# Performance work log

Hardware: AMD Instinct MI355X
Metric: run time of the kernel (lower is better)

Reference implementation:

```python
import jax, jax.numpy as jnp
import numpy as np
from math import factorial

# ---- static config mirroring Cace.__init__ ----
MAX_L = 3            # max angular degree
N_RBF = 8            # Bessel radial basis size
RB = 8               # n_radial_basis (radial embedding dim after transform)
K = 3                # n_atom_basis -> edge channels C = K*K
NZ = 4               # len(zs)
CUTOFF = 5.5
N_NODES = 2000
N_EDGES = 50000
T_MP = 1             # num_message_passing
MP_NORM = 1.0 / np.sqrt(25.0)   # 1/sqrt(avg_num_neighbors)
C = K * K

def _lxlylz(max_l):
    out = []
    for l in range(max_l + 1):
        for lx in range(l, -1, -1):
            for ly in range(l - lx, -1, -1):
                out.append((lx, ly, l - lx - ly))
    return out

L_LIST = _lxlylz(MAX_L)                 # 20 Cartesian monomials for max_l=3
NL = len(L_LIST)
LX = np.array([t[0] for t in L_LIST]); LY = np.array([t[1] for t in L_LIST]); LZ = np.array([t[2] for t in L_LIST])
DEGS = LX + LY + LZ                     # degree l of each monomial
MULTI = np.array([factorial(int(d)) / (factorial(int(a)) * factorial(int(b)) * factorial(int(c)))
                  for a, b, c, d in zip(LX, LY, LZ, DEGS)], dtype=np.float32)
SEL = np.zeros((NL, MAX_L + 1), np.float32)
SEL[np.arange(NL), DEGS] = 1.0          # monomial -> degree one-hot (for per-l sums)
NB = 1 + (MAX_L + 1)                    # symmetrizer feats: nu=1 (l=0) + nu=2 per l

def bessel(r):  # [E] -> [E, N_RBF]
    n = jnp.arange(1, N_RBF + 1, dtype=r.dtype)
    return jnp.sqrt(2.0 / CUTOFF) * jnp.sin(n[None, :] * jnp.pi * r[:, None] / CUTOFF) / r[:, None]

def poly_cutoff(r):  # MACE-style polynomial cutoff, p=6
    p = 6.0
    u = r / CUTOFF
    f = 1.0 - (p + 1.0) * (p + 2.0) / 2.0 * u**6 + p * (p + 2.0) * u**7 - p * (p + 1.0) / 2.0 * u**8
    return f * (u < 1.0)

def axis_pows(x):  # [E] -> [E, MAX_L+1] = x^0..x^MAX_L (safe grads, handles negatives)
    pows = [jnp.ones_like(x)]
    for _ in range(MAX_L):
        pows.append(pows[-1] * x)
    return jnp.stack(pows, axis=1)

def angular(u):  # unit vectors [E,3] -> Cartesian monomials [E, NL]
    return axis_pows(u[:, 0])[:, LX] * axis_pows(u[:, 1])[:, LY] * axis_pows(u[:, 2])[:, LZ]

def radial_transform(x, W):  # x [N,R,L,C], W [MAX_L+1,R,Rb] shared per degree l
    return jnp.einsum('nrlc,lrb->nblc', x, W[DEGS])

def symmetrize(A):  # A [N,Rb,NL,C] -> B [N,Rb,NB,C]
    b1 = A[:, :, :1, :]  # nu=1: the (0,0,0) monomial (index 0)
    w = (A * A) * jnp.asarray(MULTI)[None, None, :, None]
    b2 = jnp.einsum('nrlc,lm->nrmc', w, jnp.asarray(SEL))  # nu=2 invariant per degree l
    return jnp.concatenate([b1, b2], axis=2)


def setup_inputs() -> dict:
    key = jax.random.key(0)
    ks = jax.random.split(key, 9)
    positions = jax.random.uniform(ks[0], (N_NODES, 3), dtype=jnp.float32) * 12.0
    species = jax.random.randint(ks[1], (N_NODES,), 0, NZ)
    send = jax.random.randint(ks[2], (N_EDGES,), 0, N_NODES)
    off = jax.random.randint(ks[3], (N_EDGES,), 1, N_NODES)
    recv = (send + off) % N_NODES  # no self-edges -> strictly positive edge lengths
    edge_index = jnp.stack([send, recv])
    shifts = jnp.zeros((N_EDGES, 3), jnp.float32)
    W_embed = jax.random.normal(ks[4], (NZ, K), jnp.float32)
    W_radial = jax.random.normal(ks[5], (MAX_L + 1, N_RBF, RB), jnp.float32) / np.sqrt(N_RBF)
    W_mem = jax.random.normal(ks[6], (MAX_L + 1, RB, RB), jnp.float32) / np.sqrt(RB)
    W_ar = jax.random.normal(ks[7], (N_RBF, RB), jnp.float32) / np.sqrt(N_RBF)
    W_chi = jax.random.normal(ks[8], (RB, NB), jnp.float32) * 0.1
    return {"positions": positions, "shifts": shifts, "W_embed": W_embed, "W_radial": W_radial,
            "W_mem": W_mem, "W_ar": W_ar, "W_chi": W_chi, "species": species, "edge_index": edge_index}


def reference(positions, shifts, W_embed, W_radial, W_mem, W_ar, W_chi, species, edge_index):
    n_nodes = positions.shape[0]
    send, recv = edge_index[0], edge_index[1]
    # edge geometry
    vec = positions[recv] - positions[send] + shifts
    lengths = jnp.linalg.norm(vec, axis=-1)
    u = vec / (lengths[:, None] + 1e-9)
    rad = bessel(lengths)          # [E,R]
    fcut = poly_cutoff(lengths)    # [E]
    ang = angular(u)               # [E,NL]
    # edge type encoding: outer product of sender/receiver species embeddings
    emb = W_embed[species]         # [N,K]
    enc = (emb[send][:, :, None] * emb[recv][:, None, :]).reshape(-1, C)  # [E,C]
    # elementwise_multiply_3tensors -> [E,R,NL,C]
    edge_attri = jnp.einsum('er,el,ec->erlc', rad * fcut[:, None], ang, enc)
    A = radial_transform(jax.ops.segment_sum(edge_attri, recv, num_segments=n_nodes), W_radial)  # [N,Rb,NL,C]
    B = symmetrize(A)              # [N,Rb,NB,C]
    feats = [B]
    for _ in range(T_MP):
        mem = jnp.einsum('nrlc,lrb->nblc', A, W_mem[DEGS])        # NodeMemory
        chi = jnp.einsum('nbkc,bk->nc', B, W_chi)                  # MessageBchi node scalar
        msg_bchi = edge_attri * chi[send][:, None, None, :]
        A_bchi = radial_transform(jax.ops.segment_sum(msg_bchi, recv, num_segments=n_nodes), W_radial)
        fr = (rad @ W_ar) * fcut[:, None]                          # MessageAr radial filter [E,Rb]
        msg_ar = A[send] * fr[:, :, None, None]
        A_ar = jax.ops.segment_sum(msg_ar, recv, num_segments=n_nodes)
        A = (A_ar + A_bchi) * MP_NORM + mem
        B = symmetrize(A)
        feats.append(B)
    return jnp.stack(feats, axis=-1)   # [N,Rb,NB,C,T_MP+1]
```

## Files before the change

kernel.cpp:

```cpp
#include <hip/hip_runtime.h>
#include <hip/hip_bf16.h>


#define CUTF 5.5f
#define MPNORM 0.2f

__constant__ int   d_DEGS[20]  = {0,1,1,1,2,2,2,2,2,2,3,3,3,3,3,3,3,3,3,3};
__constant__ float d_MULTI[20] = {1,1,1,1,1,2,2,1,2,1,1,3,3,3,6,3,1,3,3,1};

__global__ __launch_bounds__(1024) void k_prep(const int* __restrict__ eidx,
                                               int* __restrict__ offs,
                                               int* __restrict__ erank,
                                               int N, int E) {
  __shared__ int cnt[2048];
  __shared__ int part[1024];
  int t = threadIdx.x;
  cnt[t] = 0; cnt[t + 1024] = 0;
  __syncthreads();
  const int* recv = eidx + E;
  if ((E & 3) == 0) {
    for (int i = t * 4; i + 3 < E; i += 4096) {
      int4 v = *reinterpret_cast<const int4*>(recv + i);
      int r0 = atomicAdd(&cnt[v.x], 1);
      int r1 = atomicAdd(&cnt[v.y], 1);
      int r2 = atomicAdd(&cnt[v.z], 1);
      int r3 = atomicAdd(&cnt[v.w], 1);
      *reinterpret_cast<int4*>(erank + i) = make_int4(r0, r1, r2, r3);
    }
  } else {
    for (int i = t; i < E; i += 1024) erank[i] = atomicAdd(&cnt[recv[i]], 1);
  }
  __syncthreads();
  int a = cnt[2 * t], b = cnt[2 * t + 1];
  int s = a + b;
  part[t] = s;
  __syncthreads();
  for (int d = 1; d < 1024; d <<= 1) {
    int add = (t >= d) ? part[t - d] : 0;
    __syncthreads();
    part[t] += add;
    __syncthreads();
  }
  int excl = part[t] - s;
  if (2 * t     < N) offs[2 * t]     = excl;
  if (2 * t + 1 < N) offs[2 * t + 1] = excl + a;
  if (t == 1023) offs[N] = part[1023];
}

__global__ __launch_bounds__(64) void k_edge(
                       const float* __restrict__ pos,
                       const float* __restrict__ shifts,
                       const float* __restrict__ Wemb,
                       const float* __restrict__ War,
                       const int* __restrict__ species,
                       const int* __restrict__ eidx,
                       const int* __restrict__ offs,
                       const int* __restrict__ erank,
                       float* __restrict__ edata,
                       int* __restrict__ esend,
                       int E) {
  __shared__ float war_s[64];
  int t = threadIdx.x;
  war_s[t] = War[t];
  __syncthreads();
  int e = blockIdx.x * 64 + t;
  if (e >= E) return;
  int s  = eidx[e];
  int rI = eidx[E + e];
  int rk = erank[e];
  float vx = pos[rI*3+0] - pos[s*3+0] + shifts[e*3+0];
  float vy = pos[rI*3+1] - pos[s*3+1] + shifts[e*3+1];
  float vz = pos[rI*3+2] - pos[s*3+2] + shifts[e*3+2];
  float len = sqrtf(vx*vx + vy*vy + vz*vz);
  float inv = 1.0f / (len + 1e-9f);
  float ux = vx*inv, uy = vy*inv, uz = vz*inv;
  float uu = len * (1.0f/CUTF);
  float u2 = uu*uu, u6 = u2*u2*u2;
  float fcut = (uu < 1.0f) ? (1.0f - 28.0f*u6 + 48.0f*u6*uu - 21.0f*u6*u2) : 0.0f;
  float x = 3.14159265358979f * uu;
  float sn = sinf(x), c2 = 2.0f*cosf(x), snm1 = 0.0f;
  float pref = sqrtf(2.0f/CUTF) / (len + 1e-20f);
  float rad[8];
  float v[48];
  #pragma unroll
  for (int k = 0; k < 8; k++) {
    rad[k] = pref * sn;
    v[k]   = rad[k] * fcut;
    float nxt = c2*sn - snm1; snm1 = sn; sn = nxt;
  }
  #pragma unroll
  for (int b = 0; b < 8; b++) {
    float a = 0.0f;
    #pragma unroll
    for (int k = 0; k < 8; k++) a += rad[k] * war_s[k*8+b];
    v[8+b] = a * fcut;
  }
  float px2 = ux*ux, py2 = uy*uy, pz2 = uz*uz;
  v[16] = 1.0f; v[17] = ux;     v[18] = uy;     v[19] = uz;
  v[20] = px2;  v[21] = ux*uy;  v[22] = ux*uz;  v[23] = py2;
  v[24] = uy*uz;v[25] = pz2;
  v[26] = px2*ux; v[27] = px2*uy; v[28] = px2*uz; v[29] = ux*py2;
  v[30] = ux*uy*uz; v[31] = ux*pz2; v[32] = py2*uy; v[33] = py2*uz;
  v[34] = uy*pz2; v[35] = pz2*uz;
  int zs = species[s], zr = species[rI];
  float es0 = Wemb[zs*3+0], es1 = Wemb[zs*3+1], es2 = Wemb[zs*3+2];
  float er0 = Wemb[zr*3+0], er1 = Wemb[zr*3+1], er2 = Wemb[zr*3+2];
  v[36] = es0*er0; v[37] = es0*er1; v[38] = es0*er2;
  v[39] = es1*er0; v[40] = es1*er1; v[41] = es1*er2;
  v[42] = es2*er0; v[43] = es2*er1; v[44] = es2*er2;
  v[45] = 0.0f; v[46] = 0.0f; v[47] = 0.0f;
  int dst = offs[rI] + rk;
  float4* eb4 = reinterpret_cast<float4*>(edata + (size_t)dst * 48);
  #pragma unroll
  for (int w = 0; w < 12; w++)
    eb4[w] = make_float4(v[4*w], v[4*w+1], v[4*w+2], v[4*w+3]);
  esend[dst] = s;
}

__global__ __launch_bounds__(192) void k_nodeA(
    const float* __restrict__ edata, const int* __restrict__ offs,
    const float* __restrict__ Wrad, const float* __restrict__ Wchi,
    float* __restrict__ A, uint4* __restrict__ Abf2,
    float* __restrict__ chi, float* __restrict__ B0, int N) {
  __shared__ float wr_s[288];
  __shared__ float wchi_s[40];
  __shared__ float Bsh[2][360];
  int t = threadIdx.x;
  int n0 = blockIdx.x * 2, n1 = n0 + 1;
  for (int i = t; i < 256; i += 192) { int d = i >> 6, rm = i & 63; wr_s[d*72+rm] = Wrad[i]; }
  for (int i = t; i < 40;  i += 192) wchi_s[i] = Wchi[i];
  for (int i = t; i < 720; i += 192) (&Bsh[0][0])[i] = 0.0f;
  int l = t / 9, c = t - l*9;
  bool act = t < 180;
  int ll = act ? l : 0, cc = act ? c : 0;
  int s0 = offs[n0], m0 = offs[n0+1];
  int m1 = (n1 < N) ? offs[n0+2] : m0;
  int L0 = m0 - s0, L1 = m1 - m0;
  int Lc = (L0 < L1) ? L0 : L1;
  float acc0[8], acc1[8];
  #pragma unroll
  for (int r = 0; r < 8; r++) { acc0[r] = 0.0f; acc1[r] = 0.0f; }
  #pragma unroll 2
  for (int i = 0; i < Lc; i++) {
    const float* r0 = edata + (size_t)(s0+i) * 48;
    const float* r1 = edata + (size_t)(m0+i) * 48;
    float p0 = r0[16+ll] * r0[36+cc];
    float p1 = r1[16+ll] * r1[36+cc];
    #pragma unroll
    for (int r = 0; r < 8; r++) { acc0[r] += r0[r] * p0; acc1[r] += r1[r] * p1; }
  }
  #pragma unroll 4
  for (int i = Lc; i < L0; i++) {
    const float* r0 = edata + (size_t)(s0+i) * 48;
    float p0 = r0[16+ll] * r0[36+cc];
    #pragma unroll
    for (int r = 0; r < 8; r++) acc0[r] += r0[r] * p0;
  }
  #pragma unroll 4
  for (int i = Lc; i < L1; i++) {
    const float* r1 = edata + (size_t)(m0+i) * 48;
    float p1 = r1[16+ll] * r1[36+cc];
    #pragma unroll
    for (int r = 0; r < 8; r++) acc1[r] += r1[r] * p1;
  }
  __syncthreads();
  int deg = act ? d_DEGS[ll] : 0;
  float mlt = d_MULTI[ll]; int kk = 1 + deg;
  const float* wp = &wr_s[deg*72];
  #pragma unroll
  for (int q = 0; q < 2; q++) {
    int n = n0 + q;
    if (n >= N) break;
    const float* ac = q ? acc1 : acc0;
    float Ab[8];
    #pragma unroll
    for (int b = 0; b < 8; b++) {
      float a = 0.0f;
      #pragma unroll
      for (int r = 0; r < 8; r++) a += ac[r] * wp[r*8+b];
      Ab[b] = a;
    }
    if (act) {
      #pragma unroll
      for (int b = 0; b < 8; b++) A[(size_t)n*1440 + t*8 + b] = Ab[b];
      unsigned int pk[4];
      #pragma unroll
      for (int bp = 0; bp < 4; bp++) {
        __hip_bfloat16 blo = __float2bfloat16(Ab[2*bp]);
        __hip_bfloat16 bhi = __float2bfloat16(Ab[2*bp+1]);
        pk[bp] = (unsigned int)(*reinterpret_cast<unsigned short*>(&blo))
               | ((unsigned int)(*reinterpret_cast<unsigned short*>(&bhi)) << 16);
      }
      uint4 qv; qv.x = pk[0]; qv.y = pk[1]; qv.z = pk[2]; qv.w = pk[3];
      Abf2[(size_t)n*180 + t] = qv;
      if (l == 0) {
        #pragma unroll
        for (int b = 0; b < 8; b++) Bsh[q][b*45 + c] = Ab[b];
      }
      #pragma unroll
      for (int b = 0; b < 8; b++) atomicAdd(&Bsh[q][b*45 + kk*9 + c], mlt*Ab[b]*Ab[b]);
    }
  }
  __syncthreads();
  if (t < 18) {
    int q = t / 9, tc = t - q*9;
    int n = n0 + q;
    if (n < N) {
      float s = 0.0f;
      for (int b = 0; b < 8; b++)
        #pragma unroll
        for (int kq = 0; kq < 5; kq++) s += Bsh[q][b*45 + kq*9 + tc] * wchi_s[b*5 + kq];
      chi[n*9 + tc] = s;
    }
  }
  int tot = (n1 < N) ? 720 : 360;
  for (int i = t; i < tot; i += 192)
    B0[(size_t)n0*360 + i] = (&Bsh[0][0])[i];
}

__global__ __launch_bounds__(192) void k_node2(
    const float* __restrict__ edata, const int* __restrict__ esend,
    const int* __restrict__ offs,
    const float* __restrict__ Wrad, const float* __restrict__ Wmem,
    const float* __restrict__ A, const uint4* __restrict__ Abf2,
    const float* __restrict__ chi, const float* __restrict__ B0,
    float* __restrict__ out, int N) {
  __shared__ float wr_s[288], wm_s[288];
  __shared__ float Bsh[2][360];
  int t = threadIdx.x;
  int n0 = blockIdx.x * 2, n1 = n0 + 1;
  for (int i = t; i < 256; i += 192) {
    int d = i >> 6, rm = i & 63;
    wr_s[d*72+rm] = Wrad[i];
    wm_s[d*72+rm] = Wmem[i];
  }
  for (int i = t; i < 720; i += 192) (&Bsh[0][0])[i] = 0.0f;
  int l = t / 9, c = t - l*9;
  bool act = t < 180;
  int ll = act ? l : 0, cc = act ? c : 0;
  int tt = act ? t : 0;
  int s0 = offs[n0], m0 = offs[n0+1];
  int m1 = (n1 < N) ? offs[n0+2] : m0;
  int L0 = m0 - s0, L1 = m1 - m0;
  int Lc = (L0 < L1) ? L0 : L1;
  float S0[8], R0[8], S1[8], R1[8];
  #pragma unroll
  for (int r = 0; r < 8; r++) { S0[r]=0.0f; R0[r]=0.0f; S1[r]=0.0f; R1[r]=0.0f; }
  #pragma unroll 2
  for (int i = 0; i < Lc; i++) {
    int j0 = s0 + i, j1 = m0 + i;
    const float* r0 = edata + (size_t)j0 * 48;
    const float* r1 = edata + (size_t)j1 * 48;
    int sd0 = esend[j0], sd1 = esend[j1];
    float ch0 = chi[sd0*9 + cc], ch1 = chi[sd1*9 + cc];
    const uint4 q0 = Abf2[(size_t)sd0*180 + tt];
    const uint4 q1 = Abf2[(size_t)sd1*180 + tt];
    float pc0 = r0[16+ll] * r0[36+cc] * ch0;
    float pc1 = r1[16+ll] * r1[36+cc] * ch1;
    #pragma unroll
    for (int r = 0; r < 8; r++) { S0[r] += r0[r] * pc0; S1[r] += r1[r] * pc1; }
    float a0 = __uint_as_float(q0.x << 16), a1 = __uint_as_float(q0.x & 0xffff0000u);
    float a2 = __uint_as_float(q0.y << 16), a3 = __uint_as_float(q0.y & 0xffff0000u);
    float a4 = __uint_as_float(q0.z << 16), a5 = __uint_as_float(q0.z & 0xffff0000u);
    float a6 = __uint_as_float(q0.w << 16), a7 = __uint_as_float(q0.w & 0xffff0000u);
    R0[0] += a0*r0[8];  R0[1] += a1*r0[9];  R0[2] += a2*r0[10]; R0[3] += a3*r0[11];
    R0[4] += a4*r0[12]; R0[5] += a5*r0[13]; R0[6] += a6*r0[14]; R0[7] += a7*r0[15];
    float b0 = __uint_as_float(q1.x << 16), b1 = __uint_as_float(q1.x & 0xffff0000u);
    float b2 = __uint_as_float(q1.y << 16), b3 = __uint_as_float(q1.y & 0xffff0000u);
    float b4 = __uint_as_float(q1.z << 16), b5 = __uint_as_float(q1.z & 0xffff0000u);
    float b6 = __uint_as_float(q1.w << 16), b7 = __uint_as_float(q1.w & 0xffff0000u);
    R1[0] += b0*r1[8];  R1[1] += b1*r1[9];  R1[2] += b2*r1[10]; R1[3] += b3*r1[11];
    R1[4] += b4*r1[12]; R1[5] += b5*r1[13]; R1[6] += b6*r1[14]; R1[7] += b7*r1[15];
  }
  #pragma unroll 4
  for (int i = Lc; i < L0; i++) {
    int j0 = s0 + i;
    const float* r0 = edata + (size_t)j0 * 48;
    int sd0 = esend[j0];
    float ch0 = chi[sd0*9 + cc];
    const uint4 q0 = Abf2[(size_t)sd0*180 + tt];
    float pc0 = r0[16+ll] * r0[36+cc] * ch0;
    #pragma unroll
    for (int r = 0; r < 8; r++) S0[r] += r0[r] * pc0;
    float a0 = __uint_as_float(q0.x << 16), a1 = __uint_as_float(q0.x & 0xffff0000u);
    float a2 = __uint_as_float(q0.y << 16), a3 = __uint_as_float(q0.y & 0xffff0000u);
    float a4 = __uint_as_float(q0.z << 16), a5 = __uint_as_float(q0.z & 0xffff0000u);
    float a6 = __uint_as_float(q0.w << 16), a7 = __uint_as_float(q0.w & 0xffff0000u);
    R0[0] += a0*r0[8];  R0[1] += a1*r0[9];  R0[2] += a2*r0[10]; R0[3] += a3*r0[11];
    R0[4] += a4*r0[12]; R0[5] += a5*r0[13]; R0[6] += a6*r0[14]; R0[7] += a7*r0[15];
  }
  #pragma unroll 4
  for (int i = Lc; i < L1; i++) {
    int j1 = m0 + i;
    const float* r1 = edata + (size_t)j1 * 48;
    int sd1 = esend[j1];
    float ch1 = chi[sd1*9 + cc];
    const uint4 q1 = Abf2[(size_t)sd1*180 + tt];
    float pc1 = r1[16+ll] * r1[36+cc] * ch1;
    #pragma unroll
    for (int r = 0; r < 8; r++) S1[r] += r1[r] * pc1;
    float b0 = __uint_as_float(q1.x << 16), b1 = __uint_as_float(q1.x & 0xffff0000u);
    float b2 = __uint_as_float(q1.y << 16), b3 = __uint_as_float(q1.y & 0xffff0000u);
    float b4 = __uint_as_float(q1.z << 16), b5 = __uint_as_float(q1.z & 0xffff0000u);
    float b6 = __uint_as_float(q1.w << 16), b7 = __uint_as_float(q1.w & 0xffff0000u);
    R1[0] += b0*r1[8];  R1[1] += b1*r1[9];  R1[2] += b2*r1[10]; R1[3] += b3*r1[11];
    R1[4] += b4*r1[12]; R1[5] += b5*r1[13]; R1[6] += b6*r1[14]; R1[7] += b7*r1[15];
  }
  __syncthreads();
  int deg = act ? d_DEGS[ll] : 0;
  float mlt = d_MULTI[ll]; int kk = 1 + deg;
  const float* wrp = &wr_s[deg*72];
  const float* wmp = &wm_s[deg*72];
  #pragma unroll
  for (int q = 0; q < 2; q++) {
    int n = n0 + q;
    if (n >= N) break;
    if (act) {
      const float* Sq = q ? S1 : S0;
      const float* Rq = q ? R1 : R0;
      const float* aop = A + (size_t)n*1440 + t*8;
      float aown[8];
      #pragma unroll
      for (int r = 0; r < 8; r++) aown[r] = aop[r];
      float newA[8];
      #pragma unroll
      for (int b = 0; b < 8; b++) {
        float mem = 0.0f, ab = 0.0f;
        #pragma unroll
        for (int r = 0; r < 8; r++) { mem += aown[r]*wmp[r*8+b]; ab += Sq[r]*wrp[r*8+b]; }
        newA[b] = (Rq[b] + ab)*MPNORM + mem;
      }
      if (l == 0) {
        #pragma unroll
        for (int b = 0; b < 8; b++) Bsh[q][b*45 + c] = newA[b];
      }
      #pragma unroll
      for (int b = 0; b < 8; b++) atomicAdd(&Bsh[q][b*45 + kk*9 + c], mlt*newA[b]*newA[b]);
    }
  }
  __syncthreads();
  float2* out2 = reinterpret_cast<float2*>(out);
  int tot = (n1 < N) ? 720 : 360;
  for (int i = t; i < tot; i += 192) {
    float2 pk;
    pk.x = B0[(size_t)n0*360 + i];
    pk.y = (&Bsh[0][0])[i];
    out2[(size_t)n0*360 + i] = pk;
  }
}

extern "C" void kernel_launch(void* const* d_in, const int* in_sizes, int n_in,
                              void* d_out, int out_size, void* d_ws, size_t ws_size,
                              hipStream_t stream) {
  const float* pos    = (const float*)d_in[0];
  const float* shifts = (const float*)d_in[1];
  const float* Wemb   = (const float*)d_in[2];
  const float* Wrad   = (const float*)d_in[3];
  const float* Wmem   = (const float*)d_in[4];
  const float* War    = (const float*)d_in[5];
  const float* Wchi   = (const float*)d_in[6];
  const int* species = (const int*)d_in[7];
  const int* eidx    = (const int*)d_in[8];
  float* out = (float*)d_out;
  int N = in_sizes[7];
  int E = in_sizes[8] / 2;

  char* base = (char*)d_ws;
  size_t off = 0;
  float* edata = (float*)(base + off); off += (size_t)E*48*4;
  float* A     = (float*)(base + off); off += (size_t)N*1440*4;
  uint4* Abf2  = (uint4*)(base + off); off += (size_t)N*180*16;
  float* chi   = (float*)(base + off); off += (size_t)N*9*4;
  float* B0    = (float*)(base + off); off += (size_t)N*360*4;
  int* offs    = (int*)(base + off);   off += (((size_t)(N+1)*4) + 15) & ~(size_t)15;
  int* esend   = (int*)(base + off);   off += (size_t)E*4;
  int* erank   = (int*)(base + off);   off += (((size_t)E*4) + 15) & ~(size_t)15;

  int G = (N + 1) / 2;
  k_prep<<<1, 1024, 0, stream>>>(eidx, offs, erank, N, E);
  k_edge<<<(E + 63) / 64, 64, 0, stream>>>(pos, shifts, Wemb, War, species, eidx,
                                           offs, erank, edata, esend, E);
  k_nodeA<<<G, 192, 0, stream>>>(edata, offs, Wrad, Wchi, A, Abf2, chi, B0, N);
  k_node2<<<G, 192, 0, stream>>>(edata, esend, offs, Wrad, Wmem, A, Abf2, chi, B0, out, N);
}
```

Baseline: 150.7 us.

## Split single-block CSR prep into multi-block count kernel plus scan kernel

The receiver histogram and per-edge rank used to be computed by one 1024-thread block with shared-memory atomics, followed by a scan in the same block. That work now runs as a memset, a grid-wide kernel doing global atomics on the counts, and a separate single-block 256-thread scan with 8 elements per thread. The aim is to spread the 50k-edge counting over many CUs instead of serialising it on one. In exchange it adds two extra launches and uses slower global atomics. The new scan also covers only 2048 nodes, the same limit the old code had.

```diff
diff --git a/kernel.cpp b/kernel.cpp
--- a/kernel.cpp
+++ b/kernel.cpp
@@ -8,43 +8,36 @@
 __constant__ int   d_DEGS[20]  = {0,1,1,1,2,2,2,2,2,2,3,3,3,3,3,3,3,3,3,3};
 __constant__ float d_MULTI[20] = {1,1,1,1,1,2,2,1,2,1,1,3,3,3,6,3,1,3,3,1};
 
-__global__ __launch_bounds__(1024) void k_prep(const int* __restrict__ eidx,
-                                               int* __restrict__ offs,
-                                               int* __restrict__ erank,
-                                               int N, int E) {
-  __shared__ int cnt[2048];
-  __shared__ int part[1024];
+__global__ void k_count(const int* __restrict__ eidx, int* __restrict__ counts,
+                        int* __restrict__ erank, int E) {
+  int e = blockIdx.x * blockDim.x + threadIdx.x;
+  if (e < E) erank[e] = atomicAdd(&counts[eidx[E + e]], 1);
+}
+
+__global__ void k_scan(const int* __restrict__ counts, int* __restrict__ offs, int N) {
+  __shared__ int part[256];
   int t = threadIdx.x;
-  cnt[t] = 0; cnt[t + 1024] = 0;
-  __syncthreads();
-  const int* recv = eidx + E;
-  if ((E & 3) == 0) {
-    for (int i = t * 4; i + 3 < E; i += 4096) {
-      int4 v = *reinterpret_cast<const int4*>(recv + i);
-      int r0 = atomicAdd(&cnt[v.x], 1);
-      int r1 = atomicAdd(&cnt[v.y], 1);
-      int r2 = atomicAdd(&cnt[v.z], 1);
-      int r3 = atomicAdd(&cnt[v.w], 1);
-      *reinterpret_cast<int4*>(erank + i) = make_int4(r0, r1, r2, r3);
-    }
-  } else {
-    for (int i = t; i < E; i += 1024) erank[i] = atomicAdd(&cnt[recv[i]], 1);
-  }
-  __syncthreads();
-  int a = cnt[2 * t], b = cnt[2 * t + 1];
-  int s = a + b;
-  part[t] = s;
-  __syncthreads();
-  for (int d = 1; d < 1024; d <<= 1) {
-    int add = (t >= d) ? part[t - d] : 0;
+  int local[8]; int sum = 0;
+  #pragma unroll
+  for (int i = 0; i < 8; i++) {
+    int idx = t*8 + i;
+    int v = (idx < N) ? counts[idx] : 0;
+    local[i] = sum; sum += v;
+  }
+  part[t] = sum; __syncthreads();
+  for (int d = 1; d < 256; d <<= 1) {
+    int add = (t >= d) ? part[t-d] : 0;
     __syncthreads();
     part[t] += add;
     __syncthreads();
   }
-  int excl = part[t] - s;
-  if (2 * t     < N) offs[2 * t]     = excl;
-  if (2 * t + 1 < N) offs[2 * t + 1] = excl + a;
-  if (t == 1023) offs[N] = part[1023];
+  int excl = part[t] - sum;
+  #pragma unroll
+  for (int i = 0; i < 8; i++) {
+    int idx = t*8 + i;
+    if (idx < N) offs[idx] = excl + local[i];
+  }
+  if (t == 255) offs[N] = part[255];
 }
 
 __global__ __launch_bounds__(64) void k_edge(
@@ -372,12 +365,15 @@
   uint4* Abf2  = (uint4*)(base + off); off += (size_t)N*180*16;
   float* chi   = (float*)(base + off); off += (size_t)N*9*4;
   float* B0    = (float*)(base + off); off += (size_t)N*360*4;
+  int* counts  = (int*)(base + off);   off += (size_t)N*4;
   int* offs    = (int*)(base + off);   off += (((size_t)(N+1)*4) + 15) & ~(size_t)15;
   int* esend   = (int*)(base + off);   off += (size_t)E*4;
   int* erank   = (int*)(base + off);   off += (((size_t)E*4) + 15) & ~(size_t)15;
 
   int G = (N + 1) / 2;
-  k_prep<<<1, 1024, 0, stream>>>(eidx, offs, erank, N, E);
+  hipMemsetAsync(counts, 0, (size_t)N*4, stream);
+  k_count<<<(E + 255) / 256, 256, 0, stream>>>(eidx, counts, erank, E);
+  k_scan<<<1, 256, 0, stream>>>(counts, offs, N);
   k_edge<<<(E + 63) / 64, 64, 0, stream>>>(pos, shifts, Wemb, War, species, eidx,
                                            offs, erank, edata, esend, E);
   k_nodeA<<<G, 192, 0, stream>>>(edata, offs, Wrad, Wchi, A, Abf2, chi, B0, N);
```

After: 156.7 us. 1.04x slower.

## Recompute fp32 A and B0 in second node kernel instead of storing them

Applied to the files above, without the earlier changes.

k_nodeA no longer writes the full fp32 A tensor or B0 to global memory. k_node2 instead re-accumulates the unweighted edge sum alongside the chi-weighted sum, reapplies the radial transform to rebuild A, and symmetrizes both layers in shared memory before writing them together. This removes roughly 11.5 MB of global writes and reads in exchange for extra FMAs and registers in the edge loop plus doubled shared memory for Bsh.

```diff
diff --git a/kernel.cpp b/kernel.cpp
--- a/kernel.cpp
+++ b/kernel.cpp
@@ -120,8 +120,7 @@
 __global__ __launch_bounds__(192) void k_nodeA(
     const float* __restrict__ edata, const int* __restrict__ offs,
     const float* __restrict__ Wrad, const float* __restrict__ Wchi,
-    float* __restrict__ A, uint4* __restrict__ Abf2,
-    float* __restrict__ chi, float* __restrict__ B0, int N) {
+    uint4* __restrict__ Abf2, float* __restrict__ chi, int N) {
   __shared__ float wr_s[288];
   __shared__ float wchi_s[40];
   __shared__ float Bsh[2][360];
@@ -181,8 +180,6 @@
       Ab[b] = a;
     }
     if (act) {
-      #pragma unroll
-      for (int b = 0; b < 8; b++) A[(size_t)n*1440 + t*8 + b] = Ab[b];
       unsigned int pk[4];
       #pragma unroll
       for (int bp = 0; bp < 4; bp++) {
@@ -213,20 +210,16 @@
       chi[n*9 + tc] = s;
     }
   }
-  int tot = (n1 < N) ? 720 : 360;
-  for (int i = t; i < tot; i += 192)
-    B0[(size_t)n0*360 + i] = (&Bsh[0][0])[i];
 }
 
 __global__ __launch_bounds__(192) void k_node2(
     const float* __restrict__ edata, const int* __restrict__ esend,
     const int* __restrict__ offs,
     const float* __restrict__ Wrad, const float* __restrict__ Wmem,
-    const float* __restrict__ A, const uint4* __restrict__ Abf2,
-    const float* __restrict__ chi, const float* __restrict__ B0,
+    const uint4* __restrict__ Abf2, const float* __restrict__ chi,
     float* __restrict__ out, int N) {
   __shared__ float wr_s[288], wm_s[288];
-  __shared__ float Bsh[2][360];
+  __shared__ float Bsh[4][360];
   int t = threadIdx.x;
   int n0 = blockIdx.x * 2, n1 = n0 + 1;
   for (int i = t; i < 256; i += 192) {
@@ -234,7 +227,7 @@
     wr_s[d*72+rm] = Wrad[i];
     wm_s[d*72+rm] = Wmem[i];
   }
-  for (int i = t; i < 720; i += 192) (&Bsh[0][0])[i] = 0.0f;
+  for (int i = t; i < 1440; i += 192) (&Bsh[0][0])[i] = 0.0f;
   int l = t / 9, c = t - l*9;
   bool act = t < 180;
   int ll = act ? l : 0, cc = act ? c : 0;
@@ -243,9 +236,11 @@
   int m1 = (n1 < N) ? offs[n0+2] : m0;
   int L0 = m0 - s0, L1 = m1 - m0;
   int Lc = (L0 < L1) ? L0 : L1;
-  float S0[8], R0[8], S1[8], R1[8];
-  #pragma unroll
-  for (int r = 0; r < 8; r++) { S0[r]=0.0f; R0[r]=0.0f; S1[r]=0.0f; R1[r]=0.0f; }
+  float A0[8], A1[8], S0[8], S1[8], R0[8], R1[8];
+  #pragma unroll
+  for (int r = 0; r < 8; r++) {
+    A0[r]=0.0f; A1[r]=0.0f; S0[r]=0.0f; S1[r]=0.0f; R0[r]=0.0f; R1[r]=0.0f;
+  }
   #pragma unroll 2
   for (int i = 0; i < Lc; i++) {
     int j0 = s0 + i, j1 = m0 + i;
@@ -255,10 +250,14 @@
     float ch0 = chi[sd0*9 + cc], ch1 = chi[sd1*9 + cc];
     const uint4 q0 = Abf2[(size_t)sd0*180 + tt];
     const uint4 q1 = Abf2[(size_t)sd1*180 + tt];
-    float pc0 = r0[16+ll] * r0[36+cc] * ch0;
-    float pc1 = r1[16+ll] * r1[36+cc] * ch1;
-    #pragma unroll
-    for (int r = 0; r < 8; r++) { S0[r] += r0[r] * pc0; S1[r] += r1[r] * pc1; }
+    float p0 = r0[16+ll] * r0[36+cc];
+    float p1 = r1[16+ll] * r1[36+cc];
+    float pc0 = p0 * ch0, pc1 = p1 * ch1;
+    #pragma unroll
+    for (int r = 0; r < 8; r++) {
+      A0[r] += r0[r] * p0;  A1[r] += r1[r] * p1;
+      S0[r] += r0[r] * pc0; S1[r] += r1[r] * pc1;
+    }
     float a0 = __uint_as_float(q0.x << 16), a1 = __uint_as_float(q0.x & 0xffff0000u);
     float a2 = __uint_as_float(q0.y << 16), a3 = __uint_as_float(q0.y & 0xffff0000u);
     float a4 = __uint_as_float(q0.z << 16), a5 = __uint_as_float(q0.z & 0xffff0000u);
@@ -279,9 +278,10 @@
     int sd0 = esend[j0];
     float ch0 = chi[sd0*9 + cc];
     const uint4 q0 = Abf2[(size_t)sd0*180 + tt];
-    float pc0 = r0[16+ll] * r0[36+cc] * ch0;
-    #pragma unroll
-    for (int r = 0; r < 8; r++) S0[r] += r0[r] * pc0;
+    float p0 = r0[16+ll] * r0[36+cc];
+    float pc0 = p0 * ch0;
+    #pragma unroll
+    for (int r = 0; r < 8; r++) { A0[r] += r0[r] * p0; S0[r] += r0[r] * pc0; }
     float a0 = __uint_as_float(q0.x << 16), a1 = __uint_as_float(q0.x & 0xffff0000u);
     float a2 = __uint_as_float(q0.y << 16), a3 = __uint_as_float(q0.y & 0xffff0000u);
     float a4 = __uint_as_float(q0.z << 16), a5 = __uint_as_float(q0.z & 0xffff0000u);
@@ -296,9 +296,10 @@
     int sd1 = esend[j1];
     float ch1 = chi[sd1*9 + cc];
     const uint4 q1 = Abf2[(size_t)sd1*180 + tt];
-    float pc1 = r1[16+ll] * r1[36+cc] * ch1;
-    #pragma unroll
-    for (int r = 0; r < 8; r++) S1[r] += r1[r] * pc1;
+    float p1 = r1[16+ll] * r1[36+cc];
+    float pc1 = p1 * ch1;
+    #pragma unroll
+    for (int r = 0; r < 8; r++) { A1[r] += r1[r] * p1; S1[r] += r1[r] * pc1; }
     float b0 = __uint_as_float(q1.x << 16), b1 = __uint_as_float(q1.x & 0xffff0000u);
     float b2 = __uint_as_float(q1.y << 16), b3 = __uint_as_float(q1.y & 0xffff0000u);
     float b4 = __uint_as_float(q1.z << 16), b5 = __uint_as_float(q1.z & 0xffff0000u);
@@ -316,26 +317,37 @@
     int n = n0 + q;
     if (n >= N) break;
     if (act) {
+      const float* Aq = q ? A1 : A0;
       const float* Sq = q ? S1 : S0;
       const float* Rq = q ? R1 : R0;
-      const float* aop = A + (size_t)n*1440 + t*8;
-      float aown[8];
-      #pragma unroll
-      for (int r = 0; r < 8; r++) aown[r] = aop[r];
+      float Ab[8];
+      #pragma unroll
+      for (int b = 0; b < 8; b++) {
+        float a = 0.0f;
+        #pragma unroll
+        for (int r = 0; r < 8; r++) a += Aq[r] * wrp[r*8+b];
+        Ab[b] = a;
+      }
       float newA[8];
       #pragma unroll
       for (int b = 0; b < 8; b++) {
         float mem = 0.0f, ab = 0.0f;
         #pragma unroll
-        for (int r = 0; r < 8; r++) { mem += aown[r]*wmp[r*8+b]; ab += Sq[r]*wrp[r*8+b]; }
+        for (int r = 0; r < 8; r++) { mem += Ab[r]*wmp[r*8+b]; ab += Sq[r]*wrp[r*8+b]; }
         newA[b] = (Rq[b] + ab)*MPNORM + mem;
       }
       if (l == 0) {
         #pragma unroll
-        for (int b = 0; b < 8; b++) Bsh[q][b*45 + c] = newA[b];
-      }
-      #pragma unroll
-      for (int b = 0; b < 8; b++) atomicAdd(&Bsh[q][b*45 + kk*9 + c], mlt*newA[b]*newA[b]);
+        for (int b = 0; b < 8; b++) {
+          Bsh[q][b*45 + c] = Ab[b];
+          Bsh[2+q][b*45 + c] = newA[b];
+        }
+      }
+      #pragma unroll
+      for (int b = 0; b < 8; b++) {
+        atomicAdd(&Bsh[q][b*45 + kk*9 + c], mlt*Ab[b]*Ab[b]);
+        atomicAdd(&Bsh[2+q][b*45 + kk*9 + c], mlt*newA[b]*newA[b]);
+      }
     }
   }
   __syncthreads();
@@ -343,8 +355,8 @@
   int tot = (n1 < N) ? 720 : 360;
   for (int i = t; i < tot; i += 192) {
     float2 pk;
-    pk.x = B0[(size_t)n0*360 + i];
-    pk.y = (&Bsh[0][0])[i];
+    pk.x = (&Bsh[0][0])[i];
+    pk.y = (&Bsh[2][0])[i];
     out2[(size_t)n0*360 + i] = pk;
   }
 }
@@ -368,10 +380,8 @@
   char* base = (char*)d_ws;
   size_t off = 0;
   float* edata = (float*)(base + off); off += (size_t)E*48*4;
-  float* A     = (float*)(base + off); off += (size_t)N*1440*4;
   uint4* Abf2  = (uint4*)(base + off); off += (size_t)N*180*16;
   float* chi   = (float*)(base + off); off += (size_t)N*9*4;
-  float* B0    = (float*)(base + off); off += (size_t)N*360*4;
   int* offs    = (int*)(base + off);   off += (((size_t)(N+1)*4) + 15) & ~(size_t)15;
   int* esend   = (int*)(base + off);   off += (size_t)E*4;
   int* erank   = (int*)(base + off);   off += (((size_t)E*4) + 15) & ~(size_t)15;
@@ -380,6 +390,6 @@
   k_prep<<<1, 1024, 0, stream>>>(eidx, offs, erank, N, E);
   k_edge<<<(E + 63) / 64, 64, 0, stream>>>(pos, shifts, Wemb, War, species, eidx,
                                            offs, erank, edata, esend, E);
-  k_nodeA<<<G, 192, 0, stream>>>(edata, offs, Wrad, Wchi, A, Abf2, chi, B0, N);
-  k_node2<<<G, 192, 0, stream>>>(edata, esend, offs, Wrad, Wmem, A, Abf2, chi, B0, out, N);
-}
+  k_nodeA<<<G, 192, 0, stream>>>(edata, offs, Wrad, Wchi, Abf2, chi, N);
+  k_node2<<<G, 192, 0, stream>>>(edata, esend, offs, Wrad, Wmem, Abf2, chi, out, N);
+}
```

Result: slower. 161.8 us (+7.3%).
